# Kernel optimization log

Measured on AMD Instinct MI355X. Metric: run time of the kernel, lower is better.

The kernel has to match this reference:

```python
import jax, jax.numpy as jnp
import numpy as np

# ---- module constants (from __init__ defaults) ----
OUTPUT_BIT = 8
NBIT = 16            # self.N, fixed-point fraction bits for piecewise coeffs
EXP_BITWIDTH = 16
SEGMENTS = 16
DEGREE = 2


def _fit_pieces(x_np, s):
    """Replicates _compute_integer_coefficients (host-side, no_grad numpy path).

    Fits per-segment degree-2 polynomials to the IBERT integer-exp curve over the
    observed range of (x_int - rowmax) * s, then converts to integer fixed-point
    coefficients with N fraction bits.
    """
    x_int = np.floor(x_np.astype(np.float64) / s)
    x_int = x_int - x_int.max(axis=-1, keepdims=True)
    x_float = x_int * s
    x_lo = float(np.floor(x_float.min()))
    x_hi = min(float(np.ceil(x_float.max())), 0.0)
    xs = np.linspace(x_lo, x_hi, 10000, dtype=np.float32)
    xs_int = np.floor(xs / np.float32(s))
    # IBERT integer exp: exp(x) ~ 2^(-q) * poly(r), x = q*x0 + r, x0 = -ln2
    c0 = 0.35815147
    c1 = 0.96963238 / c0
    c2 = 1.0 / c0
    x0, n = -0.6931, 30
    x0_int = np.floor(np.float32(x0 / s))
    xi = np.maximum(xs_int, n * x0_int)
    q = np.floor(xi / x0_int)
    r = xi - x0_int * q
    b_int = np.floor(np.float32(c1 / s))
    c_int = np.floor(np.float32(c2 / s ** 2))
    z = r * (r + b_int) + c_int
    exp_int = np.clip(np.floor(z * 2.0 ** (n - q)), 0, None)
    ys = (exp_int * ((c0 * s ** 2) / 2.0 ** n)).astype(np.float32)
    bounds = np.linspace(x_lo, x_hi, SEGMENTS + 1, dtype=np.float32)
    lo_l, hi_l, cf_l = [], [], []
    for lo, hi in zip(bounds[:-1], bounds[1:]):
        m = (xs >= lo) & (xs <= hi)
        cf = np.polyfit(xs[m].astype(np.float64), ys[m].astype(np.float64), DEGREE).astype(np.float32)
        lo_l.append(np.floor(lo / s))
        hi_l.append(np.floor(hi / s))
        deg = len(cf) - 1
        cf_l.append([np.floor(np.float32(c) * s ** (deg - i) * 2.0 ** NBIT) for i, c in enumerate(cf)])
    return (np.asarray(lo_l, np.float32), np.asarray(hi_l, np.float32), np.asarray(cf_l, np.float32))


def setup_inputs() -> dict:
    key = jax.random.key(0)
    x = jax.random.normal(key, (4, 12, 1024, 1024), dtype=jnp.float32)  # [B,H,S,S] attn logits
    s = 0.01  # realistic 8-bit logit quantization scale
    lo_b, hi_b, coeffs = _fit_pieces(np.asarray(x), s)
    return {
        "x": x,
        "scaling_factor": jnp.asarray(s, dtype=jnp.float32),
        "lo_bounds": jnp.asarray(lo_b),
        "hi_bounds": jnp.asarray(hi_b),
        "coeffs": jnp.asarray(coeffs),  # [SEGMENTS, DEGREE+1], highest power first
    }


def reference(x, scaling_factor, lo_bounds, hi_bounds, coeffs):
    # quantize and shift so rowwise max -> 0 (hi_bounds kept for signature parity;
    # segments are contiguous so lo_bounds alone determines segment membership,
    # with ties at boundaries resolved to the higher segment as in the torch loop)
    x_int = jnp.floor(x / scaling_factor)
    x_int = x_int - jnp.max(x_int, axis=-1, keepdims=True)

    # piecewise polynomial int-exp: pick segment, Horner-evaluate integer coeffs
    seg = jnp.clip(jnp.searchsorted(lo_bounds, x_int, side="right") - 1, 0, SEGMENTS - 1)
    c = coeffs[seg]  # [..., DEGREE+1]
    r = c[..., 0]
    for i in range(1, DEGREE + 1):
        r = r * x_int + c[..., i]
    exp_int = jnp.maximum(r, 0.0)

    # renormalize exp to EXP_BITWIDTH bits, then integer softmax
    exp_int = jnp.floor(exp_int / 2.0 ** (30 - EXP_BITWIDTH + 1))
    exp_sum = jnp.maximum(jnp.sum(exp_int, axis=-1, keepdims=True), 1.0)
    factor = jnp.floor(2.0 ** 32 / exp_sum)
    softmax_int = jnp.floor(exp_int * factor / 2.0 ** (32 - OUTPUT_BIT + 1))

    softmax_float = jax.nn.softmax(x, axis=-1)
    s_out = jnp.float32(2.0 / 2.0 ** OUTPUT_BIT)
    si = softmax_int * s_out
    # straight-through combine, then re-quantize to the output grid
    output = jax.lax.stop_gradient(si) + (softmax_float - jax.lax.stop_gradient(softmax_float))
    output = s_out * jnp.floor(output / s_out)
    return output, jnp.array([s_out], dtype=x.dtype)
```

## Files before the change

kernel.cpp:

```cpp
#include <hip/hip_runtime.h>


constexpr int ROW = 1024;
constexpr int WPB = 4;
constexpr int TSIZE = 2048;

typedef float f32x4 __attribute__((ext_vector_type(4)));

__device__ __forceinline__ float eval_e(float xv,
                                        const float* __restrict__ lo,
                                        const float4* __restrict__ cf) {
    int seg = 0;
#pragma unroll
    for (int j = 1; j < 16; ++j) seg += (xv >= lo[j]) ? 1 : 0;
    const float4 c = cf[seg];
    float r = __fadd_rn(__fmul_rn(c.x, xv), c.y);
    r = __fadd_rn(__fmul_rn(r, xv), c.z);
    return floorf(fmaxf(r, 0.0f) * (1.0f / 32768.0f));
}

__global__ __launch_bounds__(256) void build_etab_kernel(
    const float* __restrict__ lo_bounds,
    const float* __restrict__ coeffs,
    float* __restrict__ gtab)
{
    const int i = blockIdx.x * 256 + threadIdx.x;
    if (i >= TSIZE) return;
    float lo[16];
    float4 cf[16];
#pragma unroll
    for (int j = 0; j < 16; ++j) {
        lo[j] = lo_bounds[j];
        cf[j] = make_float4(coeffs[j*3+0], coeffs[j*3+1], coeffs[j*3+2], 0.0f);
    }
    gtab[i] = eval_e((float)(i - (TSIZE - 1)), lo, cf);
}

template <bool LOAD_TAB>
__global__ __launch_bounds__(256) void intsoftmax_kernel(
    const float* __restrict__ x,
    const float* __restrict__ s_ptr,
    const float* __restrict__ lo_bounds,
    const float* __restrict__ coeffs,
    const float* __restrict__ gtab,
    float* __restrict__ out,
    int rows)
{
    __shared__ float etab[TSIZE];
    const int tid = threadIdx.x;

    if (LOAD_TAB) {
        const f32x4* __restrict__ gt = (const f32x4*)gtab;
        f32x4* lt = (f32x4*)etab;
        lt[tid]       = gt[tid];
        lt[tid + 256] = gt[tid + 256];
    } else {
        float lo[16];
        float4 cf[16];
#pragma unroll
        for (int j = 0; j < 16; ++j) {
            lo[j] = lo_bounds[j];
            cf[j] = make_float4(coeffs[j*3+0], coeffs[j*3+1], coeffs[j*3+2], 0.0f);
        }
        for (int i = tid; i < TSIZE; i += 256)
            etab[i] = eval_e((float)(i - (TSIZE - 1)), lo, cf);
    }
    __syncthreads();

    if (blockIdx.x == 0 && tid == 0) {
        out[(size_t)rows * ROW] = 0.0078125f;
    }

    const float s = s_ptr[0];
    const float rcp = __fdiv_rn(1.0f, s);

    const int wave = tid >> 6;
    const int lane = tid & 63;
    const long long row = (long long)blockIdx.x * WPB + wave;
    if (row >= rows) return;

    const float4* __restrict__ xr = (const float4*)(x + row * (long long)ROW);

    float xi[16];
#pragma unroll
    for (int c4 = 0; c4 < 4; ++c4) {
        const float4 v = xr[c4 * 64 + lane];
        {
            const float q0 = __fmul_rn(v.x, rcp);
            xi[c4*4+0] = floorf(__builtin_fmaf(__builtin_fmaf(-s, q0, v.x), rcp, q0));
        }
        {
            const float q0 = __fmul_rn(v.y, rcp);
            xi[c4*4+1] = floorf(__builtin_fmaf(__builtin_fmaf(-s, q0, v.y), rcp, q0));
        }
        {
            const float q0 = __fmul_rn(v.z, rcp);
            xi[c4*4+2] = floorf(__builtin_fmaf(__builtin_fmaf(-s, q0, v.z), rcp, q0));
        }
        {
            const float q0 = __fmul_rn(v.w, rcp);
            xi[c4*4+3] = floorf(__builtin_fmaf(__builtin_fmaf(-s, q0, v.w), rcp, q0));
        }
    }

    float m = xi[0];
#pragma unroll
    for (int k = 1; k < 16; ++k) m = fmaxf(m, xi[k]);
#pragma unroll
    for (int off = 32; off >= 1; off >>= 1)
        m = fmaxf(m, __shfl_xor(m, off, 64));

    const int base = (TSIZE - 1) - (int)m;
    int idx[16];
    int imin = TSIZE;
#pragma unroll
    for (int k = 0; k < 16; ++k) {
        idx[k] = (int)xi[k] + base;
        imin = min(imin, idx[k]);
    }

    float e[16];
    float psum = 0.0f;
    if (__builtin_expect(!__any(imin < 0), 1)) {
#pragma unroll
        for (int k = 0; k < 16; ++k) {
            e[k] = etab[idx[k]];
            psum += e[k];
        }
    } else {
        float lo[16];
        float4 cf[16];
#pragma unroll
        for (int j = 0; j < 16; ++j) {
            lo[j] = lo_bounds[j];
            cf[j] = make_float4(coeffs[j*3+0], coeffs[j*3+1], coeffs[j*3+2], 0.0f);
        }
#pragma unroll
        for (int k = 0; k < 16; ++k) {
            e[k] = eval_e(xi[k] - m, lo, cf);
            psum += e[k];
        }
    }

    float sum = psum;
#pragma unroll
    for (int off = 32; off >= 1; off >>= 1)
        sum += __shfl_xor(sum, off, 64);

    const float factor = floorf(__fdiv_rn(4294967296.0f, fmaxf(sum, 1.0f)));
    const float factor25 = factor * (1.0f / 33554432.0f);

    f32x4* const orow_v = (f32x4*)(out + row * (long long)ROW);
#pragma unroll
    for (int c4 = 0; c4 < 4; ++c4) {
        f32x4 o;
        o.x = floorf(__fmul_rn(e[c4*4+0], factor25)) * 0.0078125f;
        o.y = floorf(__fmul_rn(e[c4*4+1], factor25)) * 0.0078125f;
        o.z = floorf(__fmul_rn(e[c4*4+2], factor25)) * 0.0078125f;
        o.w = floorf(__fmul_rn(e[c4*4+3], factor25)) * 0.0078125f;
        __builtin_nontemporal_store(o, orow_v + c4 * 64 + lane);
    }
}

extern "C" void kernel_launch(void* const* d_in, const int* in_sizes, int n_in,
                              void* d_out, int out_size, void* d_ws, size_t ws_size,
                              hipStream_t stream) {
    const float* x      = (const float*)d_in[0];
    const float* s      = (const float*)d_in[1];
    const float* lo     = (const float*)d_in[2];
    const float* coeffs = (const float*)d_in[4];
    float* out = (float*)d_out;

    const int n = in_sizes[0];
    const int rows = n / ROW;
    const int blocks = (rows + WPB - 1) / WPB;

    if (ws_size >= TSIZE * sizeof(float)) {
        float* gtab = (float*)d_ws;
        hipLaunchKernelGGL(build_etab_kernel, dim3(TSIZE / 256), dim3(256), 0,
                           stream, lo, coeffs, gtab);
        hipLaunchKernelGGL(intsoftmax_kernel<true>, dim3(blocks), dim3(256), 0,
                           stream, x, s, lo, coeffs, gtab, out, rows);
    } else {
        hipLaunchKernelGGL(intsoftmax_kernel<false>, dim3(blocks), dim3(256), 0,
                           stream, x, s, lo, coeffs, (const float*)nullptr, out, rows);
    }
}
```

Before: 59.88 us.

## Replace exp table lookup with two-threshold ballot counting when table is step-valued

The table-build kernel now checks whether the quantized exp table only takes values 0, 1 and 2 as a step function, and records the two threshold positions. When that holds, the softmax kernel skips loading the 8KB table into shared memory and the per-element LDS gathers. It instead compares each element against two thresholds, gets the row sum from ballot popcounts, and writes one of three constant outputs. The table build becomes a single block, and the fallback paths stay in place for general tables, at the cost of extra min/max reductions and a global read of the flag.

```diff
diff --git a/kernel.cpp b/kernel.cpp
--- a/kernel.cpp
+++ b/kernel.cpp
@@ -24,8 +24,11 @@
     const float* __restrict__ coeffs,
     float* __restrict__ gtab)
 {
-    const int i = blockIdx.x * 256 + threadIdx.x;
-    if (i >= TSIZE) return;
+    __shared__ float stab[TSIZE];
+    __shared__ int s_t1, s_t2, s_ok;
+    const int tid = threadIdx.x;
+    if (tid == 0) { s_t1 = TSIZE; s_t2 = TSIZE; s_ok = 1; }
+
     float lo[16];
     float4 cf[16];
 #pragma unroll
@@ -33,10 +36,28 @@
         lo[j] = lo_bounds[j];
         cf[j] = make_float4(coeffs[j*3+0], coeffs[j*3+1], coeffs[j*3+2], 0.0f);
     }
-    gtab[i] = eval_e((float)(i - (TSIZE - 1)), lo, cf);
-}
-
-template <bool LOAD_TAB>
+    __syncthreads();
+
+    for (int i = tid; i < TSIZE; i += 256) {
+        const float e = eval_e((float)(i - (TSIZE - 1)), lo, cf);
+        stab[i] = e;
+        gtab[i] = e;
+        if (e >= 1.0f) atomicMin(&s_t1, i);
+        if (e >= 2.0f) atomicMin(&s_t2, i);
+    }
+    __syncthreads();
+    for (int i = tid; i < TSIZE; i += 256) {
+        const float want = (float)((i >= s_t1 ? 1 : 0) + (i >= s_t2 ? 1 : 0));
+        if (stab[i] != want) s_ok = 0;
+    }
+    __syncthreads();
+    if (tid == 0) {
+        gtab[TSIZE + 0] = (float)(s_t1 - (TSIZE - 1));
+        gtab[TSIZE + 1] = (float)(s_t2 - (TSIZE - 1));
+        gtab[TSIZE + 2] = (float)s_ok;
+    }
+}
+
 __global__ __launch_bounds__(256) void intsoftmax_kernel(
     const float* __restrict__ x,
     const float* __restrict__ s_ptr,
@@ -49,23 +70,15 @@
     __shared__ float etab[TSIZE];
     const int tid = threadIdx.x;
 
-    if (LOAD_TAB) {
+    const float okf = gtab[TSIZE + 2];
+    const bool fast = (okf != 0.0f);
+    if (!fast) {
         const f32x4* __restrict__ gt = (const f32x4*)gtab;
         f32x4* lt = (f32x4*)etab;
         lt[tid]       = gt[tid];
         lt[tid + 256] = gt[tid + 256];
-    } else {
-        float lo[16];
-        float4 cf[16];
-#pragma unroll
-        for (int j = 0; j < 16; ++j) {
-            lo[j] = lo_bounds[j];
-            cf[j] = make_float4(coeffs[j*3+0], coeffs[j*3+1], coeffs[j*3+2], 0.0f);
-        }
-        for (int i = tid; i < TSIZE; i += 256)
-            etab[i] = eval_e((float)(i - (TSIZE - 1)), lo, cf);
-    }
-    __syncthreads();
+        __syncthreads();
+    }
 
     if (blockIdx.x == 0 && tid == 0) {
         out[(size_t)rows * ROW] = 0.0078125f;
@@ -73,6 +86,8 @@
 
     const float s = s_ptr[0];
     const float rcp = __fdiv_rn(1.0f, s);
+    const float t1off = gtab[TSIZE + 0];
+    const float t2off = gtab[TSIZE + 1];
 
     const int wave = tid >> 6;
     const int lane = tid & 63;
@@ -81,84 +96,107 @@
 
     const float4* __restrict__ xr = (const float4*)(x + row * (long long)ROW);
 
-    float xi[16];
+    float q[16];
 #pragma unroll
     for (int c4 = 0; c4 < 4; ++c4) {
         const float4 v = xr[c4 * 64 + lane];
         {
             const float q0 = __fmul_rn(v.x, rcp);
-            xi[c4*4+0] = floorf(__builtin_fmaf(__builtin_fmaf(-s, q0, v.x), rcp, q0));
+            q[c4*4+0] = __builtin_fmaf(__builtin_fmaf(-s, q0, v.x), rcp, q0);
         }
         {
             const float q0 = __fmul_rn(v.y, rcp);
-            xi[c4*4+1] = floorf(__builtin_fmaf(__builtin_fmaf(-s, q0, v.y), rcp, q0));
+            q[c4*4+1] = __builtin_fmaf(__builtin_fmaf(-s, q0, v.y), rcp, q0);
         }
         {
             const float q0 = __fmul_rn(v.z, rcp);
-            xi[c4*4+2] = floorf(__builtin_fmaf(__builtin_fmaf(-s, q0, v.z), rcp, q0));
+            q[c4*4+2] = __builtin_fmaf(__builtin_fmaf(-s, q0, v.z), rcp, q0);
         }
         {
             const float q0 = __fmul_rn(v.w, rcp);
-            xi[c4*4+3] = floorf(__builtin_fmaf(__builtin_fmaf(-s, q0, v.w), rcp, q0));
-        }
-    }
-
-    float m = xi[0];
-#pragma unroll
-    for (int k = 1; k < 16; ++k) m = fmaxf(m, xi[k]);
-#pragma unroll
-    for (int off = 32; off >= 1; off >>= 1)
-        m = fmaxf(m, __shfl_xor(m, off, 64));
-
-    const int base = (TSIZE - 1) - (int)m;
-    int idx[16];
-    int imin = TSIZE;
-#pragma unroll
-    for (int k = 0; k < 16; ++k) {
-        idx[k] = (int)xi[k] + base;
-        imin = min(imin, idx[k]);
-    }
-
-    float e[16];
-    float psum = 0.0f;
-    if (__builtin_expect(!__any(imin < 0), 1)) {
+            q[c4*4+3] = __builtin_fmaf(__builtin_fmaf(-s, q0, v.w), rcp, q0);
+        }
+    }
+
+    float mx = q[0], mn = q[0];
+#pragma unroll
+    for (int k = 1; k < 16; ++k) { mx = fmaxf(mx, q[k]); mn = fminf(mn, q[k]); }
+#pragma unroll
+    for (int off = 32; off >= 1; off >>= 1) {
+        const float tx = __shfl_xor(mx, off, 64);
+        const float tn = __shfl_xor(mn, off, 64);
+        mx = fmaxf(mx, tx);
+        mn = fminf(mn, tn);
+    }
+    const float m = floorf(mx);
+    const bool inrange = ((int)floorf(mn) - (int)m) + (TSIZE - 1) >= 0;
+
+    f32x4* const orow_v = (f32x4*)(out + row * (long long)ROW);
+
+    if (__builtin_expect(fast && inrange, 1)) {
+        const float T1 = __fadd_rn(t1off, m);
+        const float T2 = __fadd_rn(t2off, m);
+
+        int cnt = 0;
 #pragma unroll
         for (int k = 0; k < 16; ++k) {
-            e[k] = etab[idx[k]];
-            psum += e[k];
+            cnt += __popcll(__ballot(q[k] >= T1));
+            cnt += __popcll(__ballot(q[k] >= T2));
+        }
+        const float sum = fmaxf((float)cnt, 1.0f);
+        const float factor = floorf(__fdiv_rn(4294967296.0f, sum));
+        const float f25 = factor * (1.0f / 33554432.0f);
+        const float w1 = floorf(f25) * 0.0078125f;
+        const float w2 = floorf(__fmul_rn(2.0f, f25)) * 0.0078125f;
+
+#pragma unroll
+        for (int c4 = 0; c4 < 4; ++c4) {
+            f32x4 o;
+            o.x = (q[c4*4+0] >= T1) ? ((q[c4*4+0] >= T2) ? w2 : w1) : 0.0f;
+            o.y = (q[c4*4+1] >= T1) ? ((q[c4*4+1] >= T2) ? w2 : w1) : 0.0f;
+            o.z = (q[c4*4+2] >= T1) ? ((q[c4*4+2] >= T2) ? w2 : w1) : 0.0f;
+            o.w = (q[c4*4+3] >= T1) ? ((q[c4*4+3] >= T2) ? w2 : w1) : 0.0f;
+            __builtin_nontemporal_store(o, orow_v + c4 * 64 + lane);
         }
     } else {
-        float lo[16];
-        float4 cf[16];
-#pragma unroll
-        for (int j = 0; j < 16; ++j) {
-            lo[j] = lo_bounds[j];
-            cf[j] = make_float4(coeffs[j*3+0], coeffs[j*3+1], coeffs[j*3+2], 0.0f);
-        }
-#pragma unroll
-        for (int k = 0; k < 16; ++k) {
-            e[k] = eval_e(xi[k] - m, lo, cf);
-            psum += e[k];
-        }
-    }
-
-    float sum = psum;
-#pragma unroll
-    for (int off = 32; off >= 1; off >>= 1)
-        sum += __shfl_xor(sum, off, 64);
-
-    const float factor = floorf(__fdiv_rn(4294967296.0f, fmaxf(sum, 1.0f)));
-    const float factor25 = factor * (1.0f / 33554432.0f);
-
-    f32x4* const orow_v = (f32x4*)(out + row * (long long)ROW);
-#pragma unroll
-    for (int c4 = 0; c4 < 4; ++c4) {
-        f32x4 o;
-        o.x = floorf(__fmul_rn(e[c4*4+0], factor25)) * 0.0078125f;
-        o.y = floorf(__fmul_rn(e[c4*4+1], factor25)) * 0.0078125f;
-        o.z = floorf(__fmul_rn(e[c4*4+2], factor25)) * 0.0078125f;
-        o.w = floorf(__fmul_rn(e[c4*4+3], factor25)) * 0.0078125f;
-        __builtin_nontemporal_store(o, orow_v + c4 * 64 + lane);
+        float e[16];
+        float psum = 0.0f;
+        if (!fast && inrange) {
+            const int base = (TSIZE - 1) - (int)m;
+#pragma unroll
+            for (int k = 0; k < 16; ++k) {
+                e[k] = etab[(int)floorf(q[k]) + base];
+                psum += e[k];
+            }
+        } else {
+            float lo[16];
+            float4 cf[16];
+#pragma unroll
+            for (int j = 0; j < 16; ++j) {
+                lo[j] = lo_bounds[j];
+                cf[j] = make_float4(coeffs[j*3+0], coeffs[j*3+1], coeffs[j*3+2], 0.0f);
+            }
+#pragma unroll
+            for (int k = 0; k < 16; ++k) {
+                e[k] = eval_e(floorf(q[k]) - m, lo, cf);
+                psum += e[k];
+            }
+        }
+        float sum = psum;
+#pragma unroll
+        for (int off = 32; off >= 1; off >>= 1)
+            sum += __shfl_xor(sum, off, 64);
+        const float factor = floorf(__fdiv_rn(4294967296.0f, fmaxf(sum, 1.0f)));
+        const float f25 = factor * (1.0f / 33554432.0f);
+#pragma unroll
+        for (int c4 = 0; c4 < 4; ++c4) {
+            f32x4 o;
+            o.x = floorf(__fmul_rn(e[c4*4+0], f25)) * 0.0078125f;
+            o.y = floorf(__fmul_rn(e[c4*4+1], f25)) * 0.0078125f;
+            o.z = floorf(__fmul_rn(e[c4*4+2], f25)) * 0.0078125f;
+            o.w = floorf(__fmul_rn(e[c4*4+3], f25)) * 0.0078125f;
+            __builtin_nontemporal_store(o, orow_v + c4 * 64 + lane);
+        }
     }
 }
 
@@ -175,14 +213,9 @@
     const int rows = n / ROW;
     const int blocks = (rows + WPB - 1) / WPB;
 
-    if (ws_size >= TSIZE * sizeof(float)) {
-        float* gtab = (float*)d_ws;
-        hipLaunchKernelGGL(build_etab_kernel, dim3(TSIZE / 256), dim3(256), 0,
-                           stream, lo, coeffs, gtab);
-        hipLaunchKernelGGL(intsoftmax_kernel<true>, dim3(blocks), dim3(256), 0,
-                           stream, x, s, lo, coeffs, gtab, out, rows);
-    } else {
-        hipLaunchKernelGGL(intsoftmax_kernel<false>, dim3(blocks), dim3(256), 0,
-                           stream, x, s, lo, coeffs, (const float*)nullptr, out, rows);
-    }
-}
+    float* gtab = (float*)d_ws;
+    hipLaunchKernelGGL(build_etab_kernel, dim3(1), dim3(256), 0, stream,
+                       lo, coeffs, gtab);
+    hipLaunchKernelGGL(intsoftmax_kernel, dim3(blocks), dim3(256), 0, stream,
+                       x, s, lo, coeffs, gtab, out, rows);
+}
```

Result: slower. 64.04 us (+6.9%).
